# Performance work log

Measured on AMD Instinct MI355X. Metric: run time of the kernel, lower is better.

The kernel has to match this reference:

```python
import jax, jax.numpy as jnp
import numpy as np
from jax import lax

IMG_SIZE = 608
STRIDE = 32
NUM_CLASSES = 20
CONF_THRESH = 0.001
NMS_THRESH = 0.6
SLOPE = 0.1
B = 16
P5 = 512
FMP = IMG_SIZE // STRIDE   # 19
N = FMP * FMP              # 361 boxes per image


def _conv(x, w, b):
    y = lax.conv_general_dilated(x, w, (1, 1), 'SAME',
                                 dimension_numbers=('NCHW', 'OIHW', 'NCHW'))
    return y + b[None, :, None, None]


def _conv_act(x, w, b):
    # Conv block (conv + folded-BN bias + LeakyReLU(0.1)) at inference
    return jax.nn.leaky_relu(_conv(x, w, b), SLOPE)


def _grid():
    gy, gx = jnp.meshgrid(jnp.arange(FMP), jnp.arange(FMP), indexing='ij')
    return jnp.stack([gx, gy], axis=-1).reshape(-1, 2).astype(jnp.float32)  # [N,2]


def _decode(reg):
    # reg: [B,N,4] raw head output -> normalized x1y1x2y2 clamped to [0,1]
    xy = jax.nn.sigmoid(reg[..., :2]) + _grid()[None]          # center_sample=False
    wh = jnp.exp(reg[..., 2:])
    box = jnp.concatenate([xy - wh * 0.5, xy + wh * 0.5], axis=-1)
    return jnp.clip(box * (STRIDE / IMG_SIZE), 0.0, 1.0)


def _nms_one_class(boxes, s):
    # boxes: [N,4]; s: [N] scores with -1 marking boxes not of this class / below conf
    order = jnp.argsort(-s)
    b = boxes[order]
    valid = s[order] >= CONF_THRESH
    x1, y1, x2, y2 = b[:, 0], b[:, 1], b[:, 2], b[:, 3]
    areas = (x2 - x1) * (y2 - y1)
    w = jnp.maximum(1e-28, jnp.minimum(x2[:, None], x2[None, :]) - jnp.maximum(x1[:, None], x1[None, :]))
    h = jnp.maximum(1e-28, jnp.minimum(y2[:, None], y2[None, :]) - jnp.maximum(y1[:, None], y1[None, :]))
    inter = w * h
    iou = inter / (areas[:, None] + areas[None, :] - inter + 1e-14)  # [N,N]
    later = jnp.arange(N)[None, :] > jnp.arange(N)[:, None]
    sup = (iou > NMS_THRESH) & later

    def body(i, keep):
        # box i suppresses later boxes only if itself still kept (greedy NMS)
        return keep & ~(sup[i] & keep[i])

    keep = lax.fori_loop(0, N, body, valid)
    return jnp.zeros(N, dtype=bool).at[order].set(keep)  # back to original order


def _postprocess(boxes, scores):
    # per image: boxes [N,4], scores [N,C]
    cls_inds = jnp.argmax(scores, axis=-1)
    sc = jnp.max(scores, axis=-1)
    cmask = (cls_inds[None, :] == jnp.arange(NUM_CLASSES)[:, None]) & (sc >= CONF_THRESH)[None, :]
    masked = jnp.where(cmask, sc[None, :], -1.0)  # [C,N]
    keep_c = jax.vmap(_nms_one_class, in_axes=(None, 0))(boxes, masked)
    return sc, cls_inds, jnp.any(keep_c, axis=0)


def setup_inputs() -> dict:
    key = jax.random.key(0)
    ks = jax.random.split(key, 16)
    inp = {'x': jax.random.normal(ks[0], (B, P5, FMP, FMP), jnp.float32)}
    names = ['cls1', 'cls2', 'reg1', 'reg2', 'reg3', 'reg4']
    for j, nm in enumerate(names):
        inp['w_' + nm] = jax.random.normal(ks[1 + j], (P5, P5, 3, 3), jnp.float32) * 0.02
        inp['b_' + nm] = jnp.zeros((P5,), jnp.float32)
    inp['w_obj'] = jax.random.normal(ks[8], (1, P5, 1, 1), jnp.float32) * 0.01
    inp['b_obj'] = jnp.zeros((1,), jnp.float32)
    inp['w_clsh'] = jax.random.normal(ks[9], (NUM_CLASSES, P5, 1, 1), jnp.float32) * 0.01
    inp['b_clsh'] = jnp.zeros((NUM_CLASSES,), jnp.float32)
    inp['w_regh'] = jax.random.normal(ks[10], (4, P5, 1, 1), jnp.float32) * 0.01
    inp['b_regh'] = jnp.zeros((4,), jnp.float32)
    return inp


def reference(x, w_cls1, b_cls1, w_cls2, b_cls2, w_reg1, b_reg1, w_reg2, b_reg2,
              w_reg3, b_reg3, w_reg4, b_reg4, w_obj, b_obj, w_clsh, b_clsh,
              w_regh, b_regh):
    cf = _conv_act(_conv_act(x, w_cls1, b_cls1), w_cls2, b_cls2)
    rf = x
    for wv, bv in ((w_reg1, b_reg1), (w_reg2, b_reg2), (w_reg3, b_reg3), (w_reg4, b_reg4)):
        rf = _conv_act(rf, wv, bv)

    def flat(t):  # [B,C,H,W] -> [B,N,C]
        return t.reshape(t.shape[0], t.shape[1], -1).transpose(0, 2, 1)

    obj = flat(_conv(rf, w_obj, b_obj))      # [B,N,1]
    clsp = flat(_conv(cf, w_clsh, b_clsh))   # [B,N,C]
    regp = flat(_conv(rf, w_regh, b_regh))   # [B,N,4]

    boxes = _decode(regp)                                        # [B,N,4]
    scores = jax.nn.sigmoid(obj) * jax.nn.softmax(clsp, axis=-1)  # [B,N,C]
    sc, cls_inds, keep = jax.vmap(_postprocess)(boxes, scores)
    # fixed-shape outputs: boxes [B,N,4], per-box best score [B,N],
    # class index [B,N], NMS keep mask [B,N]
    return boxes, sc, cls_inds, keep
```

## Files before the change

### kernel.cpp

```cpp
#include <hip/hip_runtime.h>
#include <hip/hip_bf16.h>
#include <stdint.h>

typedef __bf16 bf16x8 __attribute__((ext_vector_type(8)));
typedef float  f32x16 __attribute__((ext_vector_type(16)));

#define FMPX 19
#define NPOS 361
#define CCH  512
#define NB   16
#define NCLS 20
#define CONF_T 0.001f
#define NMS_TH 0.6f
#define BSCALE (32.0f/608.0f)

#define SC_OFF   (NB*NPOS*4)
#define CLS_OFF  (SC_OFF + NB*NPOS)
#define KEEP_OFF (CLS_OFF + NB*NPOS)

#define GSTR  3528
#define PLANE ((size_t)3612672)
#define WSL   294912
#define XBUF  16384
#define WBUF  18432
#define WOFF  32768
#define SMEMB 69632

__device__ __forceinline__ void gl_lds16(const void* g, void* l) {
  __builtin_amdgcn_global_load_lds(
      (const __attribute__((address_space(1))) unsigned int*)g,
      (__attribute__((address_space(3))) unsigned int*)l, 16, 0, 0);
}
#define MFMA32(A,B,C) __builtin_amdgcn_mfma_f32_32x32x16_bf16(A,B,C,0,0,0)
#define SG(m,n) __builtin_amdgcn_sched_group_barrier(m, n, 0)
#define PRIO1 __builtin_amdgcn_s_setprio(1)
#define PRIO0 __builtin_amdgcn_s_setprio(0)

__global__ void split_x_k(const float* __restrict__ x, __bf16* __restrict__ Xd) {
  __shared__ float sx[8][368];
  int g = blockIdx.x, b = blockIdx.y;
  int tid = threadIdx.x;
  for (int i = tid; i < 8*361; i += 256) {
    int ci = i / 361, p = i - ci*361;
    sx[ci][p] = x[((size_t)b*CCH + g*8 + ci)*NPOS + p];
  }
  __syncthreads();
  for (int row = tid; row < 441; row += 256) {
    int y = row/21, xx = row - y*21;
    bf16x8 oh = {}, om = {};
    if (y >= 1 && y <= 19 && xx >= 1 && xx <= 19) {
      int p = (y-1)*19 + xx - 1;
#pragma unroll
      for (int j = 0; j < 8; ++j) {
        float v = sx[j][p];
        __bf16 hh = (__bf16)v;
        oh[j] = hh; om[j] = (__bf16)(v - (float)hh);
      }
    }
    size_t o = (((size_t)b)*64 + g)*GSTR + (size_t)row*8;
    *(bf16x8*)(Xd + o)         = oh;
    *(bf16x8*)(Xd + PLANE + o) = om;
  }
}

__global__ void repack_k(const float* __restrict__ w, __bf16* __restrict__ Wg) {
  __shared__ float sw[32][145];
  int slice = blockIdx.x, chunk = blockIdx.y;
  int tid = threadIdx.x;
  for (int i = tid; i < 32*144; i += 256) {
    int cl = i / 144, r = i - cl*144;
    sw[cl][r] = w[((size_t)slice*32 + cl)*4608 + chunk*144 + r];
  }
  __syncthreads();
  for (int u = tid; u < 1152; u += 256) {
    int co = u & 31, kh = (u >> 5) & 1, pt = u >> 6;
    int tap = pt % 9, pl = pt / 9;
    bf16x8 o;
#pragma unroll
    for (int j = 0; j < 8; ++j) {
      float v = sw[co][(kh*8 + j)*9 + tap];
      __bf16 hh = (__bf16)v;
      o[j] = pl == 0 ? hh : (__bf16)(v - (float)hh);
    }
    *(bf16x8*)(Wg + (((size_t)(slice*2 + pl)*9 + tap)*32 + chunk)*512 + kh*256 + co*8) = o;
  }
}

#define RD6X(SP, AT, IMM) do { \
  SP##0 = *(const bf16x8*)(Xc + AT##0 + (IMM)); \
  SP##1 = *(const bf16x8*)(Xc + AT##1 + (IMM)); \
  SP##2 = *(const bf16x8*)(Xc + AT##2 + (IMM)); \
  SP##3 = *(const bf16x8*)(Xc + AT##3 + (IMM)); \
  SP##4 = *(const bf16x8*)(Xc + AT##4 + (IMM)); \
  SP##5 = *(const bf16x8*)(Xc + AT##5 + (IMM)); } while (0)

#define CL(SP, BH_, BM_) do { \
  acc0 = MFMA32(SP##0, BH_, acc0); acc1 = MFMA32(SP##1, BH_, acc1); \
  acc2 = MFMA32(SP##2, BH_, acc2); acc3 = MFMA32(SP##3, BH_, acc3); \
  acc4 = MFMA32(SP##4, BH_, acc4); acc5 = MFMA32(SP##5, BH_, acc5); \
  acc0 = MFMA32(SP##0, BM_, acc0); acc1 = MFMA32(SP##1, BM_, acc1); \
  acc2 = MFMA32(SP##2, BM_, acc2); acc3 = MFMA32(SP##3, BM_, acc3); \
  acc4 = MFMA32(SP##4, BM_, acc4); acc5 = MFMA32(SP##5, BM_, acc5); } while (0)

#define CLH(SP, B_) do { \
  acc0 = MFMA32(SP##0, B_, acc0); acc1 = MFMA32(SP##1, B_, acc1); \
  acc2 = MFMA32(SP##2, B_, acc2); acc3 = MFMA32(SP##3, B_, acc3); \
  acc4 = MFMA32(SP##4, B_, acc4); acc5 = MFMA32(SP##5, B_, acc5); } while (0)

#define STO(A, MTL) do { _Pragma("unroll") \
  for (int r = 0; r < 16; ++r) { \
    Lf[wq*3456 + ((MTL)*32 + 4*kh + (r & 3) + 8*(r >> 2))*36 + col] = (A)[r]; } } while (0)

__global__ __launch_bounds__(256, 2) void conv3x3_mfma(
    const __bf16* __restrict__ Xs, const __bf16* __restrict__ Wg,
    const float* __restrict__ bias, __bf16* __restrict__ Xd)
{
  __shared__ __attribute__((aligned(16))) char smem[SMEMB];
  const int tid = threadIdx.x;
  const int bid = blockIdx.x;
  const int b = bid & 15, slice = (bid >> 4) & 15, h = bid >> 8;
  const int lane = tid & 63;
  const int wq = __builtin_amdgcn_readfirstlane(tid >> 6);
  const int col = lane & 31, kh = lane >> 5;
  const int kh4096 = kh*4096;
  const int PB = h*190, CNT = h ? 171 : 190;
  const int PEND = PB + CNT - 1;
  const int clampU = h ? 230 : 251;

  int ab0, ab1, ab2, ab3, ab4, ab5;
  {
    int ao[6];
#pragma unroll
    for (int mt = 0; mt < 6; ++mt) {
      int p = PB + mt*32 + col; if (p > PEND) p = PEND;
      int pp = p + 2*(p/19) + 22;
      ao[mt] = (pp - h*210)*16;
    }
    ab0 = ao[0]; ab1 = ao[1]; ab2 = ao[2]; ab3 = ao[3]; ab4 = ao[4]; ab5 = ao[5];
  }
  const int boff = kh*512 + col*16;

  const int goffs[9] = {-352,-336,-320,-16,0,16,320,336,352};
  const int t0 = 2*wq, t1 = t0 + 1;
  const int g0 = goffs[t0], g1 = goffs[t1];
  const int a8im = 352 + ((wq & 2) ? 8192 : 0);
  const int t0a0 = ab0+g0, t0a1 = ab1+g0, t0a2 = ab2+g0,
            t0a3 = ab3+g0, t0a4 = ab4+g0, t0a5 = ab5+g0;
  const int t1a0 = ab0+g1, t1a1 = ab1+g1, t1a2 = ab2+g1,
            t1a3 = ab3+g1, t1a4 = ab4+g1, t1a5 = ab5+g1;
  const int t8a0 = ab0+a8im, t8a1 = ab1+a8im, t8a2 = ab2+a8im,
            t8a3 = ab3+a8im, t8a4 = ab4+a8im, t8a5 = ab5+a8im;
  const int wb0 = t0*1024 + boff, wb1 = t1*1024 + boff;
  const int wb8 = 8192 + boff + ((wq & 1) ? 9216 : 0);

  int ux = wq*64 + lane; if (ux > clampU) ux = clampU;
  const __bf16* xsb = Xs + (size_t)b*64*GSTR + (size_t)(h*210 + ux)*8;
  const __bf16* wsb = Wg + (size_t)slice*WSL + (size_t)lane*8;
  int wsrc0, wsrc1, wsrc2, wsrc3, wsrc4;
  int wdst0, wdst1, wdst2, wdst3, wdst4;
  {
    int ws[5], wd[5];
#pragma unroll
    for (int q = 0; q < 5; ++q) {
      int wk = (wq*5 + q) % 18;
      int pl = wk > 8 ? 1 : 0, tap = wk - 9*pl;
      ws[q] = ((pl*9 + tap)*32)*512;
      wd[q] = WOFF + pl*9216 + tap*1024;
    }
    wsrc0 = ws[0]; wsrc1 = ws[1]; wsrc2 = ws[2]; wsrc3 = ws[3]; wsrc4 = ws[4];
    wdst0 = wd[0]; wdst1 = wd[1]; wdst2 = wd[2]; wdst3 = wd[3]; wdst4 = wd[4];
  }

  auto stage = [&](int c1, int buf) {
    const __bf16* xs = xsb + (size_t)(2*c1)*GSTR;
    char* xd = smem + (buf ? XBUF : 0) + wq*1024;
    gl_lds16(xs,                    xd);
    gl_lds16(xs + GSTR,             xd + 4096);
    gl_lds16(xs + PLANE,            xd + 8192);
    gl_lds16(xs + PLANE + GSTR,     xd + 12288);
    const __bf16* wsc = wsb + (size_t)c1*512;
    char* wb = smem + (buf ? WBUF : 0);
    gl_lds16(wsc + wsrc0, wb + wdst0);
    gl_lds16(wsc + wsrc1, wb + wdst1);
    gl_lds16(wsc + wsrc2, wb + wdst2);
    gl_lds16(wsc + wsrc3, wb + wdst3);
    gl_lds16(wsc + wsrc4, wb + wdst4);
  };

  f32x16 acc0 = {}, acc1 = {}, acc2 = {}, acc3 = {}, acc4 = {}, acc5 = {};

  stage(0, 0);
  __syncthreads();

  for (int c = 0; c < 32; ++c) {
    const char* Xc = smem + (c & 1)*XBUF + kh4096;
    const char* Wc = smem + WOFF + (c & 1)*WBUF;
    const int cn = (c < 31) ? (c + 1) : 31;

    bf16x8 A00, A01, A02, A03, A04, A05;
    bf16x8 A10, A11, A12, A13, A14, A15;
    bf16x8 B0h, B0m, B1h, B1m, B8v;

    RD6X(A0, t0a, 0);
    B0h = *(const bf16x8*)(Wc + wb0);
    B0m = *(const bf16x8*)(Wc + wb0 + 9216);
    stage(cn, (c + 1) & 1);
    PRIO1;
    RD6X(A1, t0a, 8192);
    CL(A0, B0h, B0m);
    RD6X(A0, t1a, 0);
    B1h = *(const bf16x8*)(Wc + wb1);
    B1m = *(const bf16x8*)(Wc + wb1 + 9216);
    CL(A1, B0h, B0m);
    RD6X(A1, t1a, 8192);
    CL(A0, B1h, B1m);
    RD6X(A0, t8a, 0);
    B8v = *(const bf16x8*)(Wc + wb8);
    CL(A1, B1h, B1m);
    CLH(A0, B8v);
    PRIO0;

    SG(0x100, 8);
    SG(0x70, 9);
#pragma unroll
    for (int i = 0; i < 6; ++i) { SG(8, 2); SG(0x100, 1); }
#pragma unroll
    for (int i = 0; i < 4; ++i) { SG(8, 3); SG(0x100, 2); }
#pragma unroll
    for (int i = 0; i < 6; ++i) { SG(8, 2); SG(0x100, 1); }
#pragma unroll
    for (int i = 0; i < 7; ++i) { SG(8, 1); SG(0x100, 1); }
    SG(8, 11);
    __syncthreads();
  }

  float* Lf = (float*)smem;
#pragma unroll
  for (int half = 0; half < 2; ++half) {
    if (half == 0) { STO(acc0, 0); STO(acc1, 1); STO(acc2, 2); }
    else           { STO(acc3, 0); STO(acc4, 1); STO(acc5, 2); }
    __syncthreads();
    for (int u = tid; u < 768; u += 256) {
      int pl = u / 384, rem = u - pl*384;
      int gq = rem / 96, lp = rem - gq*96;
      int lpos = half*96 + lp;
      if (lpos < CNT) {
        int p = PB + lpos;
        int pp = p + 2*(p/19) + 22;
        const float* bb = bias + slice*32 + gq*8;
        bf16x8 o;
#pragma unroll
        for (int j = 0; j < 8; ++j) {
          int coix = lp*36 + gq*8 + j;
          float v = Lf[coix] + Lf[3456 + coix] + Lf[6912 + coix] + Lf[10368 + coix] + bb[j];
          v = v > 0.f ? v : 0.1f*v;
          __bf16 hh = (__bf16)v;
          o[j] = pl == 0 ? hh : (__bf16)(v - (float)hh);
        }
        *(bf16x8*)(Xd + (((size_t)pl*16 + b)*64 + slice*4 + gq)*GSTR + (size_t)pp*8) = o;
      }
    }
    __syncthreads();
  }

  const int nh = h ? 39 : 41;
  for (int u = tid; u < 8*nh; u += 256) {
    int pl = u / (4*nh); int rem = u - pl*4*nh;
    int gq = rem / nh; int ci2 = rem - gq*nh;
    int rowpos;
    if (ci2 < 21) rowpos = h ? (420 + ci2) : ci2;
    else { int q = ci2 - 21; rowpos = ((h ? 11 : 1) + (q >> 1))*21 + 20*(q & 1); }
    bf16x8 z = {};
    *(bf16x8*)(Xd + (((size_t)pl*16 + b)*64 + slice*4 + gq)*GSTR + (size_t)rowpos*8) = z;
  }
}

__global__ __launch_bounds__(256) void head_rf_k(
    const __bf16* __restrict__ F, const float* __restrict__ wobj,
    const float* __restrict__ bobj, const float* __restrict__ wreg,
    const float* __restrict__ breg, float* __restrict__ obj, float* __restrict__ regp)
{
  int gw = blockIdx.x*4 + (threadIdx.x >> 6);
  if (gw >= NB*NPOS) return;
  int lane = threadIdx.x & 63;
  int b = gw / NPOS, p = gw % NPOS;
  int pp = p + 2*(p/19) + 22;
  const __bf16* base = F + (((size_t)b)*64 + lane)*GSTR + (size_t)pp*8;
  bf16x8 v0 = *(const bf16x8*)base;
  bf16x8 v1 = *(const bf16x8*)(base + PLANE);
  float f[8];
#pragma unroll
  for (int j = 0; j < 8; ++j) f[j] = (float)v0[j] + (float)v1[j];
#pragma unroll
  for (int o = 0; o < 5; ++o) {
    const float* wp = (o == 0) ? wobj : wreg + (o-1)*CCH;
    float4 wa = *(const float4*)(wp + lane*8);
    float4 wb = *(const float4*)(wp + lane*8 + 4);
    float s2 = f[0]*wa.x + f[1]*wa.y + f[2]*wa.z + f[3]*wa.w
             + f[4]*wb.x + f[5]*wb.y + f[6]*wb.z + f[7]*wb.w;
#pragma unroll
    for (int d = 32; d; d >>= 1) s2 += __shfl_xor(s2, d);
    if (lane == 0) {
      if (o == 0) obj[gw] = s2 + bobj[0];
      else regp[(size_t)gw*4 + (o-1)] = s2 + breg[o-1];
    }
  }
}

__global__ __launch_bounds__(256) void head_cls_k(
    const __bf16* __restrict__ F, const float* __restrict__ wcls,
    const float* __restrict__ bcls, float* __restrict__ clsp)
{
  int gw = blockIdx.x*4 + (threadIdx.x >> 6);
  if (gw >= NB*NPOS) return;
  int lane = threadIdx.x & 63;
  int b = gw / NPOS, p = gw % NPOS;
  int pp = p + 2*(p/19) + 22;
  const __bf16* base = F + (((size_t)b)*64 + lane)*GSTR + (size_t)pp*8;
  bf16x8 v0 = *(const bf16x8*)base;
  bf16x8 v1 = *(const bf16x8*)(base + PLANE);
  float f[8];
#pragma unroll
  for (int j = 0; j < 8; ++j) f[j] = (float)v0[j] + (float)v1[j];
#pragma unroll
  for (int o = 0; o < NCLS; ++o) {
    const float* wp = wcls + o*CCH;
    float4 wa = *(const float4*)(wp + lane*8);
    float4 wb = *(const float4*)(wp + lane*8 + 4);
    float s2 = f[0]*wa.x + f[1]*wa.y + f[2]*wa.z + f[3]*wa.w
             + f[4]*wb.x + f[5]*wb.y + f[6]*wb.z + f[7]*wb.w;
#pragma unroll
    for (int d = 32; d; d >>= 1) s2 += __shfl_xor(s2, d);
    if (lane == 0) clsp[(size_t)gw*NCLS + o] = s2 + bcls[o];
  }
}

__global__ void decode_k(const float* __restrict__ obj, const float* __restrict__ clsp,
                         const float* __restrict__ regp, float* __restrict__ outb)
{
  int i = blockIdx.x * 256 + threadIdx.x;
  if (i >= NB * NPOS) return;
  int p = i % NPOS;
  float gx = (float)(p % FMPX), gy = (float)(p / FMPX);
  float4 rg = *(const float4*)&regp[(size_t)i * 4];
  float cx = 1.f / (1.f + expf(-rg.x)) + gx;
  float cy = 1.f / (1.f + expf(-rg.y)) + gy;
  float whw = expf(rg.z), whh = expf(rg.w);
  float x1 = fminf(fmaxf((cx - whw * 0.5f) * BSCALE, 0.f), 1.f);
  float y1 = fminf(fmaxf((cy - whh * 0.5f) * BSCALE, 0.f), 1.f);
  float x2 = fminf(fmaxf((cx + whw * 0.5f) * BSCALE, 0.f), 1.f);
  float y2 = fminf(fmaxf((cy + whh * 0.5f) * BSCALE, 0.f), 1.f);
  outb[(size_t)i * 4 + 0] = x1; outb[(size_t)i * 4 + 1] = y1;
  outb[(size_t)i * 4 + 2] = x2; outb[(size_t)i * 4 + 3] = y2;

  float so = 1.f / (1.f + expf(-obj[i]));
  float cv[20];
  const float4* cp = (const float4*)&clsp[(size_t)i * 20];
#pragma unroll
  for (int q = 0; q < 5; q++) {
    float4 v4 = cp[q];
    cv[q * 4] = v4.x; cv[q * 4 + 1] = v4.y; cv[q * 4 + 2] = v4.z; cv[q * 4 + 3] = v4.w;
  }
  float mx = cv[0];
#pragma unroll
  for (int c = 1; c < 20; c++) mx = fmaxf(mx, cv[c]);
  float sum = 0.f;
#pragma unroll
  for (int c = 0; c < 20; c++) { cv[c] = expf(cv[c] - mx); sum += cv[c]; }
  float inv = so / sum;
  float best = -1.f; int bi = 0;
#pragma unroll
  for (int c = 0; c < 20; c++) { float s = cv[c] * inv; if (s > best) { best = s; bi = c; } }
  outb[SC_OFF + i] = best;
  outb[CLS_OFF + i] = (float)bi;
  outb[KEEP_OFF + i] = 0.f;
}

__device__ inline unsigned ordf(float f) {
  unsigned u = __float_as_uint(f);
  return (u & 0x80000000u) ? ~u : (u | 0x80000000u);
}

__global__ __launch_bounds__(64) void nms_k(const float* __restrict__ outb, float* __restrict__ keep_out)
{
  int b = blockIdx.x / NCLS, c = blockIdx.x % NCLS;
  int lane = threadIdx.x;
  __shared__ unsigned long long keys[512];
  __shared__ float bx1[384], by1[384], bx2[384], by2[384], bar[384];
  __shared__ unsigned kp[384];
  __shared__ int sj[384];

  for (int i = lane; i < 512; i += 64) {
    unsigned long long key = 0ULL;
    if (i < NPOS) {
      float sc = outb[SC_OFF + b * NPOS + i];
      int ci = (int)outb[CLS_OFF + b * NPOS + i];
      float s = (ci == c && sc >= CONF_T) ? sc : -1.0f;
      key = ((unsigned long long)ordf(s) << 32) | (unsigned)(~(unsigned)i);
    }
    keys[i] = key;
  }
  __syncthreads();
  for (int kk = 2; kk <= 512; kk <<= 1) {
    for (int jj = kk >> 1; jj > 0; jj >>= 1) {
      for (int i = lane; i < 512; i += 64) {
        int l2 = i ^ jj;
        if (l2 > i) {
          unsigned long long a = keys[i], bb2 = keys[l2];
          bool dir = (i & kk) == 0;
          bool sw = dir ? (a < bb2) : (a > bb2);
          if (sw) { keys[i] = bb2; keys[l2] = a; }
        }
      }
      __syncthreads();
    }
  }
  unsigned ordc = ordf(CONF_T);
  int nvalid = 0;
  for (int i = lane; i < 384; i += 64) {
    unsigned long long key = keys[i];
    unsigned hi = (unsigned)(key >> 32);
    int j = (int)(~(unsigned)key);
    bool valid = (key != 0ULL) && (hi >= ordc);
    kp[i] = valid ? 1u : 0u;
    if (valid) {
      const float* bp = &outb[(size_t)(b * NPOS + j) * 4];
      float x1 = bp[0], y1 = bp[1], x2 = bp[2], y2 = bp[3];
      bx1[i] = x1; by1[i] = y1; bx2[i] = x2; by2[i] = y2;
      bar[i] = (x2 - x1) * (y2 - y1);
      sj[i] = j;
    } else { bx1[i] = 0; by1[i] = 0; bx2[i] = 0; by2[i] = 0; bar[i] = 0; sj[i] = 0; }
    nvalid += __popcll(__ballot(valid));
  }
  __syncthreads();
  for (int i = 0; i < nvalid; ++i) {
    if (kp[i]) {
      float x1i = bx1[i], y1i = by1[i], x2i = bx2[i], y2i = by2[i], ai = bar[i];
      for (int j2 = i + 1 + lane; j2 < nvalid; j2 += 64) {
        if (kp[j2]) {
          float ww = fmaxf(1e-28f, fminf(x2i, bx2[j2]) - fmaxf(x1i, bx1[j2]));
          float hh = fmaxf(1e-28f, fminf(y2i, by2[j2]) - fmaxf(y1i, by1[j2]));
          float inter = ww * hh;
          float iou = inter / (ai + bar[j2] - inter + 1e-14f);
          if (iou > NMS_TH) kp[j2] = 0u;
        }
      }
    }
    __syncthreads();
  }
  for (int i = lane; i < 384; i += 64)
    if (kp[i]) keep_out[b * NPOS + sj[i]] = 1.0f;
}

extern "C" void kernel_launch(void* const* d_in, const int* in_sizes, int n_in,
                              void* d_out, int out_size, void* d_ws, size_t ws_size,
                              hipStream_t stream)
{
  const float* x      = (const float*)d_in[0];
  const float* w_cls1 = (const float*)d_in[1];  const float* b_cls1 = (const float*)d_in[2];
  const float* w_cls2 = (const float*)d_in[3];  const float* b_cls2 = (const float*)d_in[4];
  const float* w_reg1 = (const float*)d_in[5];  const float* b_reg1 = (const float*)d_in[6];
  const float* w_reg2 = (const float*)d_in[7];  const float* b_reg2 = (const float*)d_in[8];
  const float* w_reg3 = (const float*)d_in[9];  const float* b_reg3 = (const float*)d_in[10];
  const float* w_reg4 = (const float*)d_in[11]; const float* b_reg4 = (const float*)d_in[12];
  const float* w_obj  = (const float*)d_in[13]; const float* b_obj  = (const float*)d_in[14];
  const float* w_clsh = (const float*)d_in[15]; const float* b_clsh = (const float*)d_in[16];
  const float* w_regh = (const float*)d_in[17]; const float* b_regh = (const float*)d_in[18];
  float* outb = (float*)d_out;

  __bf16* XsA = (__bf16*)d_ws;
  __bf16* XsB = XsA + 2*PLANE;
  __bf16* Wg  = XsB + 2*PLANE;
  float* obj  = (float*)(Wg + (size_t)16*WSL);
  float* regp = obj + NB*NPOS;
  float* clsp = regp + (size_t)NB*NPOS*4;

  auto conv = [&](const float* wsrc, const float* bsrc, const __bf16* src, __bf16* dst) {
    repack_k<<<dim3(16, 32), 256, 0, stream>>>(wsrc, Wg);
    conv3x3_mfma<<<512, 256, 0, stream>>>(src, Wg, bsrc, dst);
  };

  split_x_k<<<dim3(64, NB), 256, 0, stream>>>(x, XsA);
  conv(w_reg1, b_reg1, XsA, XsB);
  conv(w_reg2, b_reg2, XsB, XsA);
  conv(w_reg3, b_reg3, XsA, XsB);
  conv(w_reg4, b_reg4, XsB, XsA);
  head_rf_k<<<1444, 256, 0, stream>>>(XsA, w_obj, b_obj, w_regh, b_regh, obj, regp);
  split_x_k<<<dim3(64, NB), 256, 0, stream>>>(x, XsB);
  conv(w_cls1, b_cls1, XsB, XsA);
  conv(w_cls2, b_cls2, XsA, XsB);
  head_cls_k<<<1444, 256, 0, stream>>>(XsB, w_clsh, b_clsh, clsp);
  decode_k<<<(NB * NPOS + 255) / 256, 256, 0, stream>>>(obj, clsp, regp, outb);
  nms_k<<<NB * NCLS, 64, 0, stream>>>(outb, outb + KEEP_OFF);
}
```

Baseline: 680.4 us.

## Triple-buffer A fragments, pad epilogue LDS stride, reuse split input buffer

The conv inner loop now holds three sets of A fragments instead of two, so more LDS reads are issued ahead of the MFMAs, and the sched_group_barrier pattern is rebalanced to match. The epilogue LDS staging stride changes from 36 to 37 floats to avoid bank conflicts. A third workspace buffer keeps the split input alive, so the second split_x_k launch is dropped. The extra fragment registers raise VGPR pressure, which could hurt the two-blocks-per-CU occupancy target.

```diff
diff --git a/kernel.cpp b/kernel.cpp
--- a/kernel.cpp
+++ b/kernel.cpp
@@ -109,7 +109,7 @@
 
 #define STO(A, MTL) do { _Pragma("unroll") \
   for (int r = 0; r < 16; ++r) { \
-    Lf[wq*3456 + ((MTL)*32 + 4*kh + (r & 3) + 8*(r >> 2))*36 + col] = (A)[r]; } } while (0)
+    Lf[wq*3552 + ((MTL)*32 + 4*kh + (r & 3) + 8*(r >> 2))*37 + col] = (A)[r]; } } while (0)
 
 __global__ __launch_bounds__(256, 2) void conv3x3_mfma(
     const __bf16* __restrict__ Xs, const __bf16* __restrict__ Wg,
@@ -197,40 +197,40 @@
     const char* Wc = smem + WOFF + (c & 1)*WBUF;
     const int cn = (c < 31) ? (c + 1) : 31;
 
-    bf16x8 A00, A01, A02, A03, A04, A05;
-    bf16x8 A10, A11, A12, A13, A14, A15;
+    bf16x8 Aa0, Aa1, Aa2, Aa3, Aa4, Aa5;
+    bf16x8 Ab0, Ab1, Ab2, Ab3, Ab4, Ab5;
+    bf16x8 Ac0, Ac1, Ac2, Ac3, Ac4, Ac5;
     bf16x8 B0h, B0m, B1h, B1m, B8v;
 
-    RD6X(A0, t0a, 0);
+    RD6X(Aa, t0a, 0);
     B0h = *(const bf16x8*)(Wc + wb0);
     B0m = *(const bf16x8*)(Wc + wb0 + 9216);
+    RD6X(Ab, t0a, 8192);
     stage(cn, (c + 1) & 1);
     PRIO1;
-    RD6X(A1, t0a, 8192);
-    CL(A0, B0h, B0m);
-    RD6X(A0, t1a, 0);
+    RD6X(Ac, t1a, 0);
     B1h = *(const bf16x8*)(Wc + wb1);
     B1m = *(const bf16x8*)(Wc + wb1 + 9216);
-    CL(A1, B0h, B0m);
-    RD6X(A1, t1a, 8192);
-    CL(A0, B1h, B1m);
-    RD6X(A0, t8a, 0);
+    CL(Aa, B0h, B0m);
+    RD6X(Aa, t1a, 8192);
+    CL(Ab, B0h, B0m);
+    RD6X(Ab, t8a, 0);
     B8v = *(const bf16x8*)(Wc + wb8);
-    CL(A1, B1h, B1m);
-    CLH(A0, B8v);
+    CL(Ac, B1h, B1m);
+    CL(Aa, B1h, B1m);
+    CLH(Ab, B8v);
     PRIO0;
 
-    SG(0x100, 8);
+    SG(0x100, 14);
     SG(0x70, 9);
 #pragma unroll
+    for (int i = 0; i < 4; ++i) { SG(8, 3); SG(0x100, 2); }
+#pragma unroll
     for (int i = 0; i < 6; ++i) { SG(8, 2); SG(0x100, 1); }
 #pragma unroll
-    for (int i = 0; i < 4; ++i) { SG(8, 3); SG(0x100, 2); }
-#pragma unroll
-    for (int i = 0; i < 6; ++i) { SG(8, 2); SG(0x100, 1); }
-#pragma unroll
     for (int i = 0; i < 7; ++i) { SG(8, 1); SG(0x100, 1); }
-    SG(8, 11);
+    SG(8, 5);
+    SG(8, 18);
     __syncthreads();
   }
 
@@ -251,8 +251,8 @@
         bf16x8 o;
 #pragma unroll
         for (int j = 0; j < 8; ++j) {
-          int coix = lp*36 + gq*8 + j;
-          float v = Lf[coix] + Lf[3456 + coix] + Lf[6912 + coix] + Lf[10368 + coix] + bb[j];
+          int coix = lp*37 + gq*8 + j;
+          float v = Lf[coix] + Lf[3552 + coix] + Lf[7104 + coix] + Lf[10656 + coix] + bb[j];
           v = v > 0.f ? v : 0.1f*v;
           __bf16 hh = (__bf16)v;
           o[j] = pl == 0 ? hh : (__bf16)(v - (float)hh);
@@ -468,7 +468,8 @@
   const float* w_regh = (const float*)d_in[17]; const float* b_regh = (const float*)d_in[18];
   float* outb = (float*)d_out;
 
-  __bf16* XsA = (__bf16*)d_ws;
+  __bf16* Xs0 = (__bf16*)d_ws;
+  __bf16* XsA = Xs0 + 2*PLANE;
   __bf16* XsB = XsA + 2*PLANE;
   __bf16* Wg  = XsB + 2*PLANE;
   float* obj  = (float*)(Wg + (size_t)16*WSL);
@@ -480,14 +481,13 @@
     conv3x3_mfma<<<512, 256, 0, stream>>>(src, Wg, bsrc, dst);
   };
 
-  split_x_k<<<dim3(64, NB), 256, 0, stream>>>(x, XsA);
-  conv(w_reg1, b_reg1, XsA, XsB);
-  conv(w_reg2, b_reg2, XsB, XsA);
-  conv(w_reg3, b_reg3, XsA, XsB);
-  conv(w_reg4, b_reg4, XsB, XsA);
-  head_rf_k<<<1444, 256, 0, stream>>>(XsA, w_obj, b_obj, w_regh, b_regh, obj, regp);
-  split_x_k<<<dim3(64, NB), 256, 0, stream>>>(x, XsB);
-  conv(w_cls1, b_cls1, XsB, XsA);
+  split_x_k<<<dim3(64, NB), 256, 0, stream>>>(x, Xs0);
+  conv(w_reg1, b_reg1, Xs0, XsA);
+  conv(w_reg2, b_reg2, XsA, XsB);
+  conv(w_reg3, b_reg3, XsB, XsA);
+  conv(w_reg4, b_reg4, XsA, XsB);
+  head_rf_k<<<1444, 256, 0, stream>>>(XsB, w_obj, b_obj, w_regh, b_regh, obj, regp);
+  conv(w_cls1, b_cls1, Xs0, XsA);
   conv(w_cls2, b_cls2, XsA, XsB);
   head_cls_k<<<1444, 256, 0, stream>>>(XsB, w_clsh, b_clsh, clsp);
   decode_k<<<(NB * NPOS + 255) / 256, 256, 0, stream>>>(obj, clsp, regp, outb);
```

After: 679.0 us (median of 2 runs). Within noise of the previous version (-0.2%).
